# Kernel tuning notes

Hardware: AMD Instinct MI355X
Metric: run time of the kernel (lower is better)

Reference implementation:

```python
import jax, jax.numpy as jnp
import numpy as np

SLOT_DIM = 128
HIDDEN = 64


def setup_inputs() -> dict:
    key = jax.random.key(0)
    k1, k2, k3, k4, k5 = jax.random.split(key, 5)
    b, k, d, h = 64, 128, SLOT_DIM, HIDDEN
    slots = jax.random.normal(k1, (b, k, d), dtype=jnp.float32)
    # edge_mlp params: Linear(2d -> h), Linear(h -> 1)
    s1 = 1.0 / np.sqrt(2 * d)
    W1 = jax.random.uniform(k2, (h, 2 * d), minval=-s1, maxval=s1, dtype=jnp.float32)
    b1 = jax.random.uniform(k3, (h,), minval=-s1, maxval=s1, dtype=jnp.float32)
    s2 = 1.0 / np.sqrt(h)
    W2 = jax.random.uniform(k4, (h,), minval=-s2, maxval=s2, dtype=jnp.float32)
    b2 = jax.random.uniform(k5, (), minval=-s2, maxval=s2, dtype=jnp.float32)
    return {"slots": slots, "W1": W1, "b1": b1, "W2": W2, "b2": b2}


def reference(slots, W1, b1, W2, b2):
    # slots: (b,k,d). Original concatenates [left,right] along features then
    # applies Linear(2d->h). Equivalent (same math): split W1 into halves and
    # broadcast-add, avoiding the (b,k,k,2d) concat tensor.
    b, k, d = slots.shape
    left_h = jnp.einsum('bkd,hd->bkh', slots, W1[:, :d])   # (b,k,h)
    right_h = jnp.einsum('bkd,hd->bkh', slots, W1[:, d:])  # (b,k,h)
    hidden = jax.nn.relu(left_h[:, :, None, :] + right_h[:, None, :, :] + b1)  # (b,k,k,h)
    logits = jnp.einsum('bijh,h->bij', hidden, W2) + b2    # (b,k,k)
    adj = jax.nn.sigmoid(logits)
    eye = jnp.eye(k, dtype=adj.dtype)[None]
    return adj * (1.0 - eye)
```

## Files before the change

kernel.cpp:

```cpp
#include <hip/hip_runtime.h>

#define BB 64
#define KK 128
#define DD 128
#define HH 64

typedef __attribute__((ext_vector_type(8))) short bf16x8;
typedef __attribute__((ext_vector_type(4))) float f32x4;
typedef _Float16 half2v __attribute__((ext_vector_type(2)));
typedef __fp16 fp16x2 __attribute__((ext_vector_type(2)));

__device__ __forceinline__ unsigned cvt_pk_bf16(float x, float y) {
    unsigned r;
    asm("v_cvt_pk_bf16_f32 %0, %1, %2" : "=v"(r) : "v"(x), "v"(y));
    return r;
}

__device__ __forceinline__ unsigned cvt_pkrtz_u(float x, float y) {
    const fp16x2 pk = __builtin_amdgcn_cvt_pkrtz(x, y);
    return __builtin_bit_cast(unsigned, pk);
}

__device__ __forceinline__ unsigned pk_add_relu(unsigned a, unsigned b) {
    unsigned s, r;
    asm("v_pk_add_f16 %0, %1, %2" : "=v"(s) : "v"(a), "v"(b));
    asm("v_pk_max_f16 %0, %1, 0" : "=v"(r) : "v"(s));
    return r;
}

__device__ __forceinline__ float dot2acc(unsigned a, unsigned b, float c) {
#if __has_builtin(__builtin_amdgcn_fdot2)
    return __builtin_amdgcn_fdot2(__builtin_bit_cast(half2v, a),
                                  __builtin_bit_cast(half2v, b), c, false);
#else
    float r;
    asm("v_dot2_f32_f16 %0, %1, %2, %3" : "=v"(r) : "v"(a), "v"(b), "v"(c));
    return r;
#endif
}

__global__ __launch_bounds__(256) void fused_kernel(
    const float* __restrict__ slots, const float* __restrict__ W1,
    const float* __restrict__ b1, const float* __restrict__ W2,
    const float* __restrict__ b2p, float* __restrict__ out)
{
    __shared__ unsigned smem_w[16384];
    char* smem = (char*)smem_w;

    const int t   = threadIdx.x;
    const int blk = blockIdx.x;
    const int b   = blk >> 2;
    const int it  = (blk >> 1) & 1;
    const int jt  = blk & 1;

    const int lane = t & 63;
    const int w    = t >> 6;
    const int lr   = lane & 15;
    const int lk   = lane >> 4;
    const int side = w >> 1;
    const int grp  = w & 1;

    const float b1lo = (side == 0) ? b1[grp * 32 + lr]      : 0.0f;
    const float b1hi = (side == 0) ? b1[grp * 32 + 16 + lr] : 0.0f;
    float w2lo = 0.f, w2hi = 0.f;
    if (t < 32) {
        const int hl = (t & 15) + 32 * (t >> 4);
        w2lo = W2[hl]; w2hi = W2[hl + 16];
    }

    {
        const float* srcI = slots + ((size_t)(b * KK) + it * 64) * DD;
        const float* srcJ = slots + ((size_t)(b * KK) + jt * 64) * DD;
#pragma unroll
        for (int x0 = 0; x0 < 2048; x0 += 256) {
            const int x = x0 + t;
            const int row = x >> 4, cb = x & 15;
            const float* src = (row < 64 ? srcI + row * DD
                                         : srcJ + (row - 64) * DD) + cb * 8;
            const float4 f0 = *reinterpret_cast<const float4*>(src);
            const float4 f1 = *reinterpret_cast<const float4*>(src + 4);
            uint4 pk;
            pk.x = cvt_pk_bf16(f0.x, f0.y); pk.y = cvt_pk_bf16(f0.z, f0.w);
            pk.z = cvt_pk_bf16(f1.x, f1.y); pk.w = cvt_pk_bf16(f1.z, f1.w);
            *reinterpret_cast<uint4*>(smem + row * 256 + ((cb ^ (row & 7)) << 4)) = pk;
        }
#pragma unroll
        for (int x0 = 0; x0 < 2048; x0 += 256) {
            const int x = x0 + t;
            const int row = x >> 5, cb = x & 31;
            const float* src = W1 + row * 256 + cb * 8;
            const float4 f0 = *reinterpret_cast<const float4*>(src);
            const float4 f1 = *reinterpret_cast<const float4*>(src + 4);
            uint4 pk;
            pk.x = cvt_pk_bf16(f0.x, f0.y); pk.y = cvt_pk_bf16(f0.z, f0.w);
            pk.z = cvt_pk_bf16(f1.x, f1.y); pk.w = cvt_pk_bf16(f1.z, f1.w);
            *reinterpret_cast<uint4*>(smem + 32768 + row * 512 + ((cb ^ (row & 7)) << 4)) = pk;
        }
    }
    __syncthreads();

    bf16x8 af[4][4];
#pragma unroll
    for (int m = 0; m < 4; ++m)
#pragma unroll
        for (int kf = 0; kf < 4; ++kf) {
            const int row = side * 64 + 16 * m + lr;
            const int cb  = kf * 4 + lk;
            af[m][kf] = *reinterpret_cast<const bf16x8*>(
                smem + row * 256 + ((cb ^ (row & 7)) << 4));
        }
    bf16x8 bfr[2][4];
#pragma unroll
    for (int n = 0; n < 2; ++n)
#pragma unroll
        for (int kf = 0; kf < 4; ++kf) {
            const int rowB = grp * 32 + n * 16 + lr;
            const int cb   = side * 16 + kf * 4 + lk;
            bfr[n][kf] = *reinterpret_cast<const bf16x8*>(
                smem + 32768 + rowB * 512 + ((cb ^ (rowB & 7)) << 4));
        }

    f32x4 acc[4][2];
#pragma unroll
    for (int m = 0; m < 4; ++m)
#pragma unroll
        for (int n = 0; n < 2; ++n) acc[m][n] = f32x4{0.f, 0.f, 0.f, 0.f};
#pragma unroll
    for (int m = 0; m < 4; ++m)
#pragma unroll
        for (int n = 0; n < 2; ++n)
#pragma unroll
            for (int kf = 0; kf < 4; ++kf)
                acc[m][n] = __builtin_amdgcn_mfma_f32_16x16x32_bf16(
                    af[m][kf], bfr[n][kf], acc[m][n], 0, 0, 0);
    __syncthreads();

    {
        unsigned* dst = (unsigned*)smem + (side ? 2304 : 0);
#pragma unroll
        for (int m = 0; m < 4; ++m)
#pragma unroll
            for (int r = 0; r < 4; ++r) {
                const int row = 16 * m + 4 * lk + r;
                dst[row * 36 + grp * 16 + lr] =
                    cvt_pkrtz_u(acc[m][0][r] + b1lo, acc[m][1][r] + b1hi);
            }
        if (t < 32) {
            ((unsigned*)smem)[4608 + t] = cvt_pkrtz_u(w2lo, w2hi);
        }
    }
    __syncthreads();

    const int tx = t & 15;
    const int ty = t >> 4;
    const unsigned* LsP = (const unsigned*)smem;
    const unsigned* RsP = LsP + 2304;
    const unsigned* W2p = LsP + 4608;

    uint4 w2r[8];
#pragma unroll
    for (int s = 0; s < 8; ++s)
        w2r[s] = *reinterpret_cast<const uint4*>(W2p + s * 4);

    float pacc[4][4] = {};
#pragma unroll
    for (int s = 0; s < 8; ++s) {
        uint4 l4[4], r4[4];
#pragma unroll
        for (int ii = 0; ii < 4; ++ii)
            l4[ii] = *reinterpret_cast<const uint4*>(LsP + (ty + 16 * ii) * 36 + s * 4);
#pragma unroll
        for (int jj = 0; jj < 4; ++jj)
            r4[jj] = *reinterpret_cast<const uint4*>(RsP + (tx + 16 * jj) * 36 + s * 4);
#pragma unroll
        for (int ii = 0; ii < 4; ++ii)
#pragma unroll
            for (int jj = 0; jj < 4; ++jj) {
                float a = pacc[ii][jj];
                a = dot2acc(pk_add_relu(l4[ii].x, r4[jj].x), w2r[s].x, a);
                a = dot2acc(pk_add_relu(l4[ii].y, r4[jj].y), w2r[s].y, a);
                a = dot2acc(pk_add_relu(l4[ii].z, r4[jj].z), w2r[s].z, a);
                a = dot2acc(pk_add_relu(l4[ii].w, r4[jj].w), w2r[s].w, a);
                pacc[ii][jj] = a;
            }
    }

    const float b2 = *b2p;
#pragma unroll
    for (int ii = 0; ii < 4; ++ii) {
        const int gi = it * 64 + ty + 16 * ii;
        float* orow = out + ((size_t)(b * KK) + gi) * KK + jt * 64;
#pragma unroll
        for (int jj = 0; jj < 4; ++jj) {
            const int jl = tx + 16 * jj;
            const int gj = jt * 64 + jl;
            const float xv = pacc[ii][jj] + b2;
            const float sg = 1.0f / (1.0f + __expf(-xv));
            orow[jl] = (gi == gj) ? 0.0f : sg;
        }
    }
}

extern "C" void kernel_launch(void* const* d_in, const int* in_sizes, int n_in,
                              void* d_out, int out_size, void* d_ws, size_t ws_size,
                              hipStream_t stream) {
    const float* slots = (const float*)d_in[0];
    const float* W1    = (const float*)d_in[1];
    const float* b1    = (const float*)d_in[2];
    const float* W2    = (const float*)d_in[3];
    const float* b2    = (const float*)d_in[4];
    float* out = (float*)d_out;
    (void)d_ws; (void)ws_size; (void)in_sizes; (void)n_in; (void)out_size;

    fused_kernel<<<BB * 4, 256, 0, stream>>>(slots, W1, b1, W2, b2, out);
}
```

Measured before the change: 13.00 us.

## Double block size to 512 threads and split per-thread GEMM and pairwise work

Raises the block to 512 threads (8 waves) so each wave computes one 16-column hidden slice of the MFMA projection and each thread handles a 2x4 instead of 4x4 tile of output pairs. The pairwise reduction loop is software-pipelined with double-buffered LDS loads so the next step's reads overlap the current step's compute. Hidden results are now written to LDS as individual fp16 halves rather than packed pairs. More parallelism per block helps with only 256 blocks on the device, at the cost of more barrier participants and sub-word LDS stores.

```diff
diff --git a/kernel.cpp b/kernel.cpp
--- a/kernel.cpp
+++ b/kernel.cpp
@@ -3,7 +3,6 @@
 #define BB 64
 #define KK 128
 #define DD 128
-#define HH 64
 
 typedef __attribute__((ext_vector_type(8))) short bf16x8;
 typedef __attribute__((ext_vector_type(4))) float f32x4;
@@ -39,7 +38,7 @@
 #endif
 }
 
-__global__ __launch_bounds__(256) void fused_kernel(
+__global__ __launch_bounds__(512, 2) void fused_kernel(
     const float* __restrict__ slots, const float* __restrict__ W1,
     const float* __restrict__ b1, const float* __restrict__ W2,
     const float* __restrict__ b2p, float* __restrict__ out)
@@ -57,11 +56,10 @@
     const int w    = t >> 6;
     const int lr   = lane & 15;
     const int lk   = lane >> 4;
-    const int side = w >> 1;
-    const int grp  = w & 1;
-
-    const float b1lo = (side == 0) ? b1[grp * 32 + lr]      : 0.0f;
-    const float b1hi = (side == 0) ? b1[grp * 32 + 16 + lr] : 0.0f;
+    const int side = w >> 2;
+    const int hq   = w & 3;
+
+    const float badd = (side == 0) ? b1[hq * 16 + lr] : 0.0f;
     float w2lo = 0.f, w2hi = 0.f;
     if (t < 32) {
         const int hl = (t & 15) + 32 * (t >> 4);
@@ -72,7 +70,7 @@
         const float* srcI = slots + ((size_t)(b * KK) + it * 64) * DD;
         const float* srcJ = slots + ((size_t)(b * KK) + jt * 64) * DD;
 #pragma unroll
-        for (int x0 = 0; x0 < 2048; x0 += 256) {
+        for (int x0 = 0; x0 < 2048; x0 += 512) {
             const int x = x0 + t;
             const int row = x >> 4, cb = x & 15;
             const float* src = (row < 64 ? srcI + row * DD
@@ -85,7 +83,7 @@
             *reinterpret_cast<uint4*>(smem + row * 256 + ((cb ^ (row & 7)) << 4)) = pk;
         }
 #pragma unroll
-        for (int x0 = 0; x0 < 2048; x0 += 256) {
+        for (int x0 = 0; x0 < 2048; x0 += 512) {
             const int x = x0 + t;
             const int row = x >> 5, cb = x & 31;
             const float* src = W1 + row * 256 + cb * 8;
@@ -99,55 +97,42 @@
     }
     __syncthreads();
 
-    bf16x8 af[4][4];
-#pragma unroll
-    for (int m = 0; m < 4; ++m)
+    bf16x8 bfr[4];
+#pragma unroll
+    for (int kf = 0; kf < 4; ++kf) {
+        const int rowB = hq * 16 + lr;
+        const int cb   = side * 16 + kf * 4 + lk;
+        bfr[kf] = *reinterpret_cast<const bf16x8*>(
+            smem + 32768 + rowB * 512 + ((cb ^ (rowB & 7)) << 4));
+    }
+    f32x4 acc[4];
+#pragma unroll
+    for (int m = 0; m < 4; ++m) acc[m] = f32x4{0.f, 0.f, 0.f, 0.f};
+#pragma unroll
+    for (int m = 0; m < 4; ++m) {
 #pragma unroll
         for (int kf = 0; kf < 4; ++kf) {
             const int row = side * 64 + 16 * m + lr;
             const int cb  = kf * 4 + lk;
-            af[m][kf] = *reinterpret_cast<const bf16x8*>(
+            const bf16x8 af = *reinterpret_cast<const bf16x8*>(
                 smem + row * 256 + ((cb ^ (row & 7)) << 4));
-        }
-    bf16x8 bfr[2][4];
-#pragma unroll
-    for (int n = 0; n < 2; ++n)
-#pragma unroll
-        for (int kf = 0; kf < 4; ++kf) {
-            const int rowB = grp * 32 + n * 16 + lr;
-            const int cb   = side * 16 + kf * 4 + lk;
-            bfr[n][kf] = *reinterpret_cast<const bf16x8*>(
-                smem + 32768 + rowB * 512 + ((cb ^ (rowB & 7)) << 4));
-        }
-
-    f32x4 acc[4][2];
-#pragma unroll
-    for (int m = 0; m < 4; ++m)
-#pragma unroll
-        for (int n = 0; n < 2; ++n) acc[m][n] = f32x4{0.f, 0.f, 0.f, 0.f};
-#pragma unroll
-    for (int m = 0; m < 4; ++m)
-#pragma unroll
-        for (int n = 0; n < 2; ++n)
-#pragma unroll
-            for (int kf = 0; kf < 4; ++kf)
-                acc[m][n] = __builtin_amdgcn_mfma_f32_16x16x32_bf16(
-                    af[m][kf], bfr[n][kf], acc[m][n], 0, 0, 0);
+            acc[m] = __builtin_amdgcn_mfma_f32_16x16x32_bf16(af, bfr[kf], acc[m], 0, 0, 0);
+        }
+    }
     __syncthreads();
 
     {
-        unsigned* dst = (unsigned*)smem + (side ? 2304 : 0);
+        __fp16* dst = (__fp16*)smem + (side ? 4608 : 0);
+        const int g  = hq >> 1;
+        const int hl = hq & 1;
 #pragma unroll
         for (int m = 0; m < 4; ++m)
 #pragma unroll
             for (int r = 0; r < 4; ++r) {
                 const int row = 16 * m + 4 * lk + r;
-                dst[row * 36 + grp * 16 + lr] =
-                    cvt_pkrtz_u(acc[m][0][r] + b1lo, acc[m][1][r] + b1hi);
+                dst[(row * 36 + g * 16 + lr) * 2 + hl] = (__fp16)(acc[m][r] + badd);
             }
-        if (t < 32) {
-            ((unsigned*)smem)[4608 + t] = cvt_pkrtz_u(w2lo, w2hi);
-        }
+        if (t < 32) ((unsigned*)smem)[4608 + t] = cvt_pkrtz_u(w2lo, w2hi);
     }
     __syncthreads();
 
@@ -162,33 +147,45 @@
     for (int s = 0; s < 8; ++s)
         w2r[s] = *reinterpret_cast<const uint4*>(W2p + s * 4);
 
-    float pacc[4][4] = {};
-#pragma unroll
-    for (int s = 0; s < 8; ++s) {
-        uint4 l4[4], r4[4];
-#pragma unroll
-        for (int ii = 0; ii < 4; ++ii)
-            l4[ii] = *reinterpret_cast<const uint4*>(LsP + (ty + 16 * ii) * 36 + s * 4);
-#pragma unroll
-        for (int jj = 0; jj < 4; ++jj)
-            r4[jj] = *reinterpret_cast<const uint4*>(RsP + (tx + 16 * jj) * 36 + s * 4);
-#pragma unroll
-        for (int ii = 0; ii < 4; ++ii)
-#pragma unroll
-            for (int jj = 0; jj < 4; ++jj) {
-                float a = pacc[ii][jj];
-                a = dot2acc(pk_add_relu(l4[ii].x, r4[jj].x), w2r[s].x, a);
-                a = dot2acc(pk_add_relu(l4[ii].y, r4[jj].y), w2r[s].y, a);
-                a = dot2acc(pk_add_relu(l4[ii].z, r4[jj].z), w2r[s].z, a);
-                a = dot2acc(pk_add_relu(l4[ii].w, r4[jj].w), w2r[s].w, a);
-                pacc[ii][jj] = a;
-            }
-    }
+    float pacc[2][4] = {};
+    uint4 l4a[2], r4a[4], l4b[2], r4b[4];
+
+#define LD_STEP(L4, R4, s)                                                        \
+    {                                                                             \
+        _Pragma("unroll") for (int ii = 0; ii < 2; ++ii)                          \
+            L4[ii] = *reinterpret_cast<const uint4*>(LsP + (ty + 32 * ii) * 36 + (s) * 4); \
+        _Pragma("unroll") for (int jj = 0; jj < 4; ++jj)                          \
+            R4[jj] = *reinterpret_cast<const uint4*>(RsP + (tx + 16 * jj) * 36 + (s) * 4); \
+    }
+
+#define COMPUTE_STEP(L4, R4, s)                                                   \
+    {                                                                             \
+        _Pragma("unroll") for (int ii = 0; ii < 2; ++ii)                          \
+        _Pragma("unroll") for (int jj = 0; jj < 4; ++jj) {                        \
+            float a = pacc[ii][jj];                                               \
+            a = dot2acc(pk_add_relu(L4[ii].x, R4[jj].x), w2r[s].x, a);            \
+            a = dot2acc(pk_add_relu(L4[ii].y, R4[jj].y), w2r[s].y, a);            \
+            a = dot2acc(pk_add_relu(L4[ii].z, R4[jj].z), w2r[s].z, a);            \
+            a = dot2acc(pk_add_relu(L4[ii].w, R4[jj].w), w2r[s].w, a);            \
+            pacc[ii][jj] = a;                                                     \
+        }                                                                         \
+    }
+
+    LD_STEP(l4a, r4a, 0)
+#pragma unroll
+    for (int sp = 0; sp < 4; ++sp) {
+        LD_STEP(l4b, r4b, 2 * sp + 1)
+        COMPUTE_STEP(l4a, r4a, 2 * sp)
+        if (sp < 3) LD_STEP(l4a, r4a, 2 * sp + 2)
+        COMPUTE_STEP(l4b, r4b, 2 * sp + 1)
+    }
+#undef LD_STEP
+#undef COMPUTE_STEP
 
     const float b2 = *b2p;
 #pragma unroll
-    for (int ii = 0; ii < 4; ++ii) {
-        const int gi = it * 64 + ty + 16 * ii;
+    for (int ii = 0; ii < 2; ++ii) {
+        const int gi = it * 64 + ty + 32 * ii;
         float* orow = out + ((size_t)(b * KK) + gi) * KK + jt * 64;
 #pragma unroll
         for (int jj = 0; jj < 4; ++jj) {
@@ -212,5 +209,5 @@
     float* out = (float*)d_out;
     (void)d_ws; (void)ws_size; (void)in_sizes; (void)n_in; (void)out_size;
 
-    fused_kernel<<<BB * 4, 256, 0, stream>>>(slots, W1, b1, W2, b2, out);
-}
+    fused_kernel<<<BB * 4, 512, 0, stream>>>(slots, W1, b1, W2, b2, out);
+}
```

After: 12.56 us (median of 2 runs). 3.4% less time.
